# Optimization experiments

Hardware: AMD Instinct MI355X
Metric: run time of the kernel (lower is better)

## Reference

```python
import jax, jax.numpy as jnp
import numpy as np
import math

E = 512
H = 2048
P = 128  # attention_limit

def _make_params(key):
    ks = jax.random.split(key, 6)
    s = 0.02
    p = {}
    p['wq'] = jax.random.normal(ks[0], (E, E), jnp.float32) * s
    p['bq'] = jnp.zeros((E,), jnp.float32)
    p['wk'] = jax.random.normal(ks[1], (E, E), jnp.float32) * s
    p['bk'] = jnp.zeros((E,), jnp.float32)
    p['wv'] = jax.random.normal(ks[2], (E, E), jnp.float32) * s
    p['bv'] = jnp.zeros((E,), jnp.float32)
    p['w1'] = jax.random.normal(ks[3], (E, H), jnp.float32) * s
    p['b1'] = jnp.zeros((H,), jnp.float32)
    p['w2'] = jax.random.normal(ks[4], (H, E), jnp.float32) * s
    p['b2'] = jnp.zeros((E,), jnp.float32)
    p['ln1_w'] = jnp.ones((E,), jnp.float32)
    p['ln1_b'] = jnp.zeros((E,), jnp.float32)
    p['ln2_w'] = jnp.ones((E,), jnp.float32)
    p['ln2_b'] = jnp.zeros((E,), jnp.float32)
    return p

def setup_inputs() -> dict:
    key = jax.random.key(0)
    kx, kp = jax.random.split(key)
    inp = {'x': jax.random.normal(kx, (2, 1024, E), jnp.float32)}
    inp.update(_make_params(kp))
    return inp

def _layernorm(x, w, b, eps=1e-5):
    mu = jnp.mean(x, axis=-1, keepdims=True)
    var = jnp.mean((x - mu) ** 2, axis=-1, keepdims=True)
    return (x - mu) / jnp.sqrt(var + eps) * w + b

def _forward(x, wq, bq, wk, bk, wv, bv, w1, b1, w2, b2, ln1_w, ln1_b, ln2_w, ln2_b):
    B, S, Ed = x.shape
    # "RoPE" is actually additive sinusoidal PE in the source
    pos = jnp.arange(S, dtype=jnp.float32)[:, None]
    div = jnp.exp(jnp.arange(0, Ed, 2, dtype=jnp.float32) * (-math.log(10000.0) / Ed))
    pe = jnp.zeros((S, Ed), jnp.float32)
    pe = pe.at[:, 0::2].set(jnp.sin(pos * div))
    pe = pe.at[:, 1::2].set(jnp.cos(pos * div))
    x = x + pe[None]

    # local attention: pad x first, then apply K/V linears (padded rows -> bias)
    x_ext = jnp.pad(x, ((0, 0), (P, P), (0, 0)))
    q = x @ wq + bq                      # [B,S,E]
    k_ext = x_ext @ wk + bk              # [B,S+2P,E]
    v_ext = x_ext @ wv + bv
    W = 2 * P + 1
    win_idx = jnp.arange(S)[:, None] + jnp.arange(W)[None, :]  # [S,W]
    k_win = k_ext[:, win_idx]            # [B,S,W,E]
    v_win = v_ext[:, win_idx]            # [B,S,W,E]
    energy = jnp.einsum('bse,bswe->bsw', q, k_win) / jnp.sqrt(jnp.float32(Ed))
    attn = jax.nn.softmax(energy, axis=-1)
    attn_out = jnp.einsum('bsw,bswe->bse', attn, v_win)

    x = _layernorm(attn_out + x, ln1_w, ln1_b)
    ff = jnp.maximum(x @ w1 + b1, 0.0) @ w2 + b2
    return _layernorm(ff + x, ln2_w, ln2_b)

def reference(x, wq, bq, wk, bk, wv, bv, w1, b1, w2, b2, ln1_w, ln1_b, ln2_w, ln2_b):
    return _forward(x, wq, bq, wk, bk, wv, bv, w1, b1, w2, b2, ln1_w, ln1_b, ln2_w, ln2_b)
```

## Files before the change

kernel.cpp:

```cpp
#include <hip/hip_runtime.h>
#include <hip/hip_bf16.h>

#define S_LEN 1024
#define E_DIM 512
#define H_DIM 2048
#define EXTA 1296
#define BS_ROWS 2048

typedef __attribute__((ext_vector_type(8))) short bf16x8;
typedef __attribute__((ext_vector_type(4))) float f32x4;

__device__ inline ushort f2bf(float x) {
  union { float f; unsigned u; } c; c.f = x;
  unsigned u = c.u;
  u += 0x7fffu + ((u >> 16) & 1u);
  return (ushort)(u >> 16);
}
__device__ inline float bf2f(ushort u) {
  union { unsigned u; float f; } c;
  c.u = ((unsigned)u) << 16;
  return c.f;
}

__device__ inline void gload16(ushort* dst, const ushort* src) {
  __builtin_amdgcn_global_load_lds(
      (const __attribute__((address_space(1))) void*)src,
      (__attribute__((address_space(3))) void*)dst, 16, 0, 0);
}

__global__ __launch_bounds__(256) void prep_kernel(const float* __restrict__ x,
                                                   const float* __restrict__ wq,
                                                   const float* __restrict__ wk,
                                                   const float* __restrict__ wv,
                                                   const float* __restrict__ bk,
                                                   const float* __restrict__ bv,
                                                   ushort* __restrict__ xpe_bf,
                                                   ushort* __restrict__ wqkvT,
                                                   ushort* __restrict__ k_bf,
                                                   ushort* __restrict__ v_t) {
  __shared__ float t[32][33];
  const int blk = blockIdx.x;
  if (blk < 1024) {
    int idx = blk * 256 + threadIdx.x;
    int ep = idx & 255;
    int s = idx >> 8;
    int e0 = ep * 2;
    const float c = -9.210340371976184f / 512.0f;
    float freq = __expf((float)e0 * c);
    float sn, cs;
    __sincosf((float)s * freq, &sn, &cs);
    size_t base = (size_t)s * E_DIM + e0;
    float2 x0 = *(const float2*)(x + base);
    float2 x1 = *(const float2*)(x + base + S_LEN * E_DIM);
    ushort2 o0, o1;
    o0.x = f2bf(x0.x + sn); o0.y = f2bf(x0.y + cs);
    o1.x = f2bf(x1.x + sn); o1.y = f2bf(x1.y + cs);
    *(ushort2*)(xpe_bf + base) = o0;
    *(ushort2*)(xpe_bf + base + S_LEN * E_DIM) = o1;
  } else if (blk < 1792) {
    const int tile = blk - 1024;
    const int sect = tile >> 8, tt = tile & 255;
    const float* W = sect == 0 ? wq : (sect == 1 ? wk : wv);
    ushort* WT = wqkvT + (size_t)sect * 512 * 512;
    const int bx = tt & 15, by = tt >> 4;
    int lx = threadIdx.x & 31, ly = threadIdx.x >> 5;
    int n0 = bx * 32, k0 = by * 32;
#pragma unroll
    for (int r = 0; r < 4; ++r)
      t[ly + r * 8][lx] = W[(size_t)(k0 + ly + r * 8) * 512 + n0 + lx];
    __syncthreads();
#pragma unroll
    for (int r = 0; r < 4; ++r)
      WT[(size_t)(n0 + ly + r * 8) * 512 + k0 + lx] = f2bf(t[lx][ly + r * 8]);
  } else {
    int p = (blk - 1792) * 256 + threadIdx.x;
    int t2 = p / (2 * 272 * 512);
    int r2 = p % (2 * 272 * 512);
    int b = r2 / (272 * 512);
    int r3 = r2 % (272 * 512);
    if (t2 == 0) {
      int rr = r3 >> 9, e = r3 & 511;
      int row = rr < 128 ? rr : 1024 + rr;
      float v = rr < 256 ? bk[e] : 0.f;
      k_bf[((size_t)b * EXTA + row) * 512 + e] = f2bf(v);
    } else {
      int n = r3 / 272, jj = r3 % 272;
      int j = jj < 128 ? jj : 1024 + jj;
      float v = jj < 256 ? bv[n] : 0.f;
      v_t[((size_t)b * 512 + n) * EXTA + j] = f2bf(v);
    }
  }
}

__global__ __launch_bounds__(256, 4) void qkv_kernel(const ushort* __restrict__ A,
                                                     const ushort* __restrict__ Bt,
                                                     const float* __restrict__ bq,
                                                     const float* __restrict__ bk,
                                                     const float* __restrict__ bv,
                                                     ushort* __restrict__ q_out,
                                                     ushort* __restrict__ k_out,
                                                     ushort* __restrict__ v_out) {
  __shared__ ushort As[64 * 64];
  __shared__ ushort Bs[64 * 64];
  const int blk = blockIdx.x;
  const int tid = threadIdx.x;
  const int lane = tid & 63;
  const int w = tid >> 6;
  const int wr = w >> 1, wc = w & 1;
  const int l15 = lane & 15, lhi = lane >> 4;
  const int col0 = (blk % 24) * 64, row0 = (blk / 24) * 64;

  f32x4 acc[2][2] = {};

  for (int k0 = 0; k0 < 512; k0 += 64) {
#pragma unroll
    for (int it = 0; it < 2; ++it) {
      int u = it * 256 + tid;
      int r = u >> 3;
      int c16 = (u & 7) ^ (r & 7);
      gload16(&As[(size_t)u * 8], &A[(size_t)(row0 + r) * 512 + k0 + c16 * 8]);
    }
#pragma unroll
    for (int it = 0; it < 2; ++it) {
      int u = it * 256 + tid;
      int r = u >> 3;
      int c16 = (u & 7) ^ (r & 7);
      gload16(&Bs[(size_t)u * 8], &Bt[(size_t)(col0 + r) * 512 + k0 + c16 * 8]);
    }
    __syncthreads();
#pragma unroll
    for (int kk = 0; kk < 2; ++kk) {
      bf16x8 af[2], bfr[2];
#pragma unroll
      for (int mi = 0; mi < 2; ++mi) {
        int r = wr * 32 + mi * 16 + l15;
        int c16 = (kk * 4 + lhi) ^ (r & 7);
        af[mi] = *(const bf16x8*)&As[r * 64 + c16 * 8];
      }
#pragma unroll
      for (int ni = 0; ni < 2; ++ni) {
        int r = wc * 32 + ni * 16 + l15;
        int c16 = (kk * 4 + lhi) ^ (r & 7);
        bfr[ni] = *(const bf16x8*)&Bs[r * 64 + c16 * 8];
      }
#pragma unroll
      for (int mi = 0; mi < 2; ++mi)
#pragma unroll
        for (int ni = 0; ni < 2; ++ni)
          acc[mi][ni] = __builtin_amdgcn_mfma_f32_16x16x32_bf16(af[mi], bfr[ni], acc[mi][ni], 0, 0, 0);
    }
    __syncthreads();
  }

#pragma unroll
  for (int mi = 0; mi < 2; ++mi) {
    int mbase = row0 + wr * 32 + mi * 16 + lhi * 4;
#pragma unroll
    for (int ni = 0; ni < 2; ++ni) {
      int n = col0 + wc * 32 + ni * 16 + l15;
      int sect = n >> 9, nn = n & 511;
      float b = sect == 0 ? bq[nn] : (sect == 1 ? bk[nn] : bv[nn]);
      int bb = mbase >> 10;
      int s = mbase & 1023;
      if (sect == 0) {
#pragma unroll
        for (int j = 0; j < 4; ++j)
          q_out[(size_t)(mbase + j) * 512 + nn] = f2bf(acc[mi][ni][j] + b);
      } else if (sect == 1) {
#pragma unroll
        for (int j = 0; j < 4; ++j)
          k_out[((size_t)bb * EXTA + 128 + s + j) * 512 + nn] = f2bf(acc[mi][ni][j] + b);
      } else {
        ushort4 pk;
        pk.x = f2bf(acc[mi][ni][0] + b);
        pk.y = f2bf(acc[mi][ni][1] + b);
        pk.z = f2bf(acc[mi][ni][2] + b);
        pk.w = f2bf(acc[mi][ni][3] + b);
        *(ushort4*)&v_out[((size_t)bb * 512 + nn) * EXTA + 128 + s] = pk;
      }
    }
  }
}

template <int OUT>
__global__ __launch_bounds__(256, 4) void mfma_gemm(const ushort* __restrict__ A,
                                                    const ushort* __restrict__ Bt,
                                                    const float* __restrict__ bias,
                                                    void* __restrict__ Cout,
                                                    int M, int N, int K, int LDA) {
  __shared__ ushort As[64 * 64];
  __shared__ ushort Bs[64 * 64];
  const int tid = threadIdx.x;
  const int lane = tid & 63;
  const int w = tid >> 6;
  const int wr = w >> 1, wc = w & 1;
  const int l15 = lane & 15, lhi = lane >> 4;
  const int col0 = blockIdx.x * 64, row0 = blockIdx.y * 64;
  const int koff = blockIdx.z * K;

  f32x4 acc[2][2] = {};

  for (int k0 = 0; k0 < K; k0 += 64) {
#pragma unroll
    for (int it = 0; it < 2; ++it) {
      int u = it * 256 + tid;
      int r = u >> 3;
      int c16 = (u & 7) ^ (r & 7);
      gload16(&As[(size_t)u * 8], &A[(size_t)(row0 + r) * LDA + koff + k0 + c16 * 8]);
    }
#pragma unroll
    for (int it = 0; it < 2; ++it) {
      int u = it * 256 + tid;
      int r = u >> 3;
      int c16 = (u & 7) ^ (r & 7);
      gload16(&Bs[(size_t)u * 8], &Bt[(size_t)(col0 + r) * LDA + koff + k0 + c16 * 8]);
    }
    __syncthreads();
#pragma unroll
    for (int kk = 0; kk < 2; ++kk) {
      bf16x8 af[2], bfr[2];
#pragma unroll
      for (int mi = 0; mi < 2; ++mi) {
        int r = wr * 32 + mi * 16 + l15;
        int c16 = (kk * 4 + lhi) ^ (r & 7);
        af[mi] = *(const bf16x8*)&As[r * 64 + c16 * 8];
      }
#pragma unroll
      for (int ni = 0; ni < 2; ++ni) {
        int r = wc * 32 + ni * 16 + l15;
        int c16 = (kk * 4 + lhi) ^ (r & 7);
        bfr[ni] = *(const bf16x8*)&Bs[r * 64 + c16 * 8];
      }
#pragma unroll
      for (int mi = 0; mi < 2; ++mi)
#pragma unroll
        for (int ni = 0; ni < 2; ++ni)
          acc[mi][ni] = __builtin_amdgcn_mfma_f32_16x16x32_bf16(af[mi], bfr[ni], acc[mi][ni], 0, 0, 0);
    }
    __syncthreads();
  }

#pragma unroll
  for (int mi = 0; mi < 2; ++mi) {
    int mbase = row0 + wr * 32 + mi * 16 + lhi * 4;
#pragma unroll
    for (int ni = 0; ni < 2; ++ni) {
      int n = col0 + wc * 32 + ni * 16 + l15;
      if constexpr (OUT == 1) {
        float b = bias[n];
        ushort* C = (ushort*)Cout;
#pragma unroll
        for (int j = 0; j < 4; ++j)
          C[(size_t)(mbase + j) * N + n] = f2bf(fmaxf(acc[mi][ni][j] + b, 0.f));
      } else {
        float* C = (float*)Cout + (size_t)blockIdx.z * M * N;
#pragma unroll
        for (int j = 0; j < 4; ++j) C[(size_t)(mbase + j) * N + n] = acc[mi][ni][j];
      }
    }
  }
}

union AttnSm {
  struct {
    float e[16][292];
    ushort p[16][296];
    float inv[16];
    float redS[16][16];
    float redQ[16][16];
    float mu[16], rs[16];
  } a;
  float t[32][33];
};

__global__ __launch_bounds__(1024) void attn_ln1(const ushort* __restrict__ qb,
                                                 const ushort* __restrict__ kb,
                                                 const ushort* __restrict__ vt,
                                                 const ushort* __restrict__ xpe_bf,
                                                 const float* __restrict__ ln1w,
                                                 const float* __restrict__ ln1b,
                                                 const float* __restrict__ w1,
                                                 const float* __restrict__ w2,
                                                 ushort* __restrict__ w1T,
                                                 ushort* __restrict__ w2T,
                                                 ushort* __restrict__ x1bf) {
  __shared__ AttnSm sm;
  const int tid = threadIdx.x;

  if (blockIdx.x >= 128) {
    const int tile = blockIdx.x - 128;
    const float* W; ushort* WT; int K, N, bx, by;
    if (tile < 1024) {
      K = 512; N = 2048; W = w1; WT = w1T;
      bx = tile & 63; by = tile >> 6;
    } else {
      K = 2048; N = 512; W = w2; WT = w2T;
      int tt = tile - 1024; bx = tt & 15; by = tt >> 4;
    }
    int lx = tid & 31, ly = tid >> 5;
    int n0 = bx * 32, k0 = by * 32;
    sm.t[ly][lx] = W[(size_t)(k0 + ly) * N + n0 + lx];
    __syncthreads();
    WT[(size_t)(n0 + ly) * K + k0 + lx] = f2bf(sm.t[lx][ly]);
    return;
  }

  const int lane = tid & 63;
  const int w = tid >> 6;
  const int l15 = lane & 15, lhi = lane >> 4;
  const int tile = blockIdx.x;
  const int b = tile >> 6;
  const int s0 = (tile & 63) * 16;
  const int base0 = b * 1024 + s0;

  const ushort* qrow = qb + (size_t)(base0 + l15) * 512 + lhi * 8;
  bf16x8 qf[16];
#pragma unroll
  for (int ks = 0; ks < 16; ++ks) qf[ks] = *(const bf16x8*)(qrow + ks * 32);

  const float scale = 0.044194173824159216f;
  const ushort* kbase = kb + (size_t)b * EXTA * 512 + (size_t)(s0 + l15) * 512 + lhi * 8;

  for (int jt = w; jt < 18; jt += 16) {
    f32x4 acc = {};
    const ushort* kp = kbase + (size_t)jt * 16 * 512;
#pragma unroll
    for (int ks = 0; ks < 16; ++ks) {
      bf16x8 kf = *(const bf16x8*)(kp + ks * 32);
      acc = __builtin_amdgcn_mfma_f32_16x16x32_bf16(qf[ks], kf, acc, 0, 0, 0);
    }
    int jc = jt * 16 + l15;
#pragma unroll
    for (int j = 0; j < 4; ++j) {
      int i = lhi * 4 + j;
      bool valid = (jc >= i) && (jc <= i + 256);
      sm.a.e[i][jc] = valid ? acc[j] * scale : -1e30f;
    }
  }
  __syncthreads();

  {
    int r = w;
    float m = -1e30f;
#pragma unroll
    for (int t = 0; t < 5; ++t) {
      int col = lane + 64 * t;
      float e = (t < 4 || lane < 32) ? sm.a.e[r][col] : -1e30f;
      m = fmaxf(m, e);
    }
#pragma unroll
    for (int off = 1; off <= 32; off <<= 1) m = fmaxf(m, __shfl_xor(m, off));
    float s = 0.f;
#pragma unroll
    for (int t = 0; t < 5; ++t) {
      int col = lane + 64 * t;
      if (t < 4 || lane < 32) {
        float p = __expf(sm.a.e[r][col] - m);
        s += p;
        sm.a.p[r][col] = f2bf(p);
      }
    }
#pragma unroll
    for (int off = 1; off <= 32; off <<= 1) s += __shfl_xor(s, off);
    if (lane == 0) sm.a.inv[r] = 1.0f / s;
  }
  __syncthreads();

  bf16x8 pf[9];
#pragma unroll
  for (int ks = 0; ks < 9; ++ks) pf[ks] = *(const bf16x8*)&sm.a.p[l15][ks * 32 + lhi * 8];
  float inv[4];
#pragma unroll
  for (int j = 0; j < 4; ++j) inv[j] = sm.a.inv[lhi * 4 + j];

  const ushort* vbase = vt + (size_t)b * 512 * EXTA + s0 + lhi * 8;
  float val[2][4];
#pragma unroll
  for (int ni = 0; ni < 2; ++ni) {
    int n = w * 32 + ni * 16 + l15;
    f32x4 acc = {};
    const ushort* vp = vbase + (size_t)n * EXTA;
#pragma unroll
    for (int ks = 0; ks < 9; ++ks) {
      bf16x8 vf = *(const bf16x8*)(vp + ks * 32);
      acc = __builtin_amdgcn_mfma_f32_16x16x32_bf16(pf[ks], vf, acc, 0, 0, 0);
    }
#pragma unroll
    for (int j = 0; j < 4; ++j) {
      int r = lhi * 4 + j;
      val[ni][j] = acc[j] * inv[j] + bf2f(xpe_bf[(size_t)(base0 + r) * 512 + n]);
    }
  }

  float S[4], Q[4];
#pragma unroll
  for (int j = 0; j < 4; ++j) {
    S[j] = 0.f; Q[j] = 0.f;
#pragma unroll
    for (int ni = 0; ni < 2; ++ni) { S[j] += val[ni][j]; Q[j] += val[ni][j] * val[ni][j]; }
  }
#pragma unroll
  for (int off = 1; off <= 8; off <<= 1) {
#pragma unroll
    for (int j = 0; j < 4; ++j) {
      S[j] += __shfl_xor(S[j], off);
      Q[j] += __shfl_xor(Q[j], off);
    }
  }
  if (l15 == 0) {
#pragma unroll
    for (int j = 0; j < 4; ++j) { sm.a.redS[w][lhi * 4 + j] = S[j]; sm.a.redQ[w][lhi * 4 + j] = Q[j]; }
  }
  __syncthreads();
  if (tid < 16) {
    float sS = 0.f, sQ = 0.f;
#pragma unroll
    for (int ww = 0; ww < 16; ++ww) { sS += sm.a.redS[ww][tid]; sQ += sm.a.redQ[ww][tid]; }
    float mu = sS * (1.0f / 512.0f);
    float var = sQ * (1.0f / 512.0f) - mu * mu;
    sm.a.mu[tid] = mu;
    sm.a.rs[tid] = rsqrtf(var + 1e-5f);
  }
  __syncthreads();

#pragma unroll
  for (int ni = 0; ni < 2; ++ni) {
    int n = w * 32 + ni * 16 + l15;
    float lw = ln1w[n], lb = ln1b[n];
#pragma unroll
    for (int j = 0; j < 4; ++j) {
      int r = lhi * 4 + j;
      float o = (val[ni][j] - sm.a.mu[r]) * sm.a.rs[r] * lw + lb;
      x1bf[(size_t)(base0 + r) * 512 + n] = f2bf(o);
    }
  }
}

__device__ inline float wave_reduce_sum(float v) {
#pragma unroll
  for (int off = 32; off >= 1; off >>= 1) v += __shfl_xor(v, off);
  return v;
}

__global__ __launch_bounds__(256) void ln2_kernel(const float* __restrict__ parts,
                                                  const float* __restrict__ ab,
                                                  const ushort* __restrict__ rsd_bf,
                                                  const float* __restrict__ w,
                                                  const float* __restrict__ bias,
                                                  float* __restrict__ out) {
  const int row = blockIdx.x;
  const int tid = threadIdx.x;
  __shared__ float red[8];
  const int e0 = tid * 2;
  const size_t base = (size_t)row * E_DIM + e0;
  const size_t PART = (size_t)BS_ROWS * E_DIM;
  float2 v0 = *(const float2*)(parts + base);
  float2 v1 = *(const float2*)(parts + PART + base);
  float2 bb = *(const float2*)(ab + e0);
  ushort2 rv = *(const ushort2*)(rsd_bf + base);
  float x0 = v0.x + v1.x + bb.x + bf2f(rv.x);
  float x1 = v0.y + v1.y + bb.y + bf2f(rv.y);

  float sm = wave_reduce_sum(x0 + x1);
  if ((tid & 63) == 0) red[tid >> 6] = sm;
  __syncthreads();
  float mu = (red[0] + red[1] + red[2] + red[3]) * (1.0f / 512.0f);
  float d0 = x0 - mu, d1 = x1 - mu;
  float vs = wave_reduce_sum(d0 * d0 + d1 * d1);
  if ((tid & 63) == 0) red[4 + (tid >> 6)] = vs;
  __syncthreads();
  float var = (red[4] + red[5] + red[6] + red[7]) * (1.0f / 512.0f);
  float inv = rsqrtf(var + 1e-5f);
  float2 wv = *(const float2*)(w + e0);
  float2 bi = *(const float2*)(bias + e0);
  float o0 = d0 * inv * wv.x + bi.x;
  float o1 = d1 * inv * wv.y + bi.y;
  *(float2*)(out + base) = make_float2(o0, o1);
}

extern "C" void kernel_launch(void* const* d_in, const int* in_sizes, int n_in,
                              void* d_out, int out_size, void* d_ws, size_t ws_size,
                              hipStream_t stream) {
  const float* x    = (const float*)d_in[0];
  const float* wq   = (const float*)d_in[1];
  const float* bq   = (const float*)d_in[2];
  const float* wk   = (const float*)d_in[3];
  const float* bk   = (const float*)d_in[4];
  const float* wv   = (const float*)d_in[5];
  const float* bv   = (const float*)d_in[6];
  const float* w1   = (const float*)d_in[7];
  const float* b1   = (const float*)d_in[8];
  const float* w2   = (const float*)d_in[9];
  const float* b2   = (const float*)d_in[10];
  const float* ln1w = (const float*)d_in[11];
  const float* ln1b = (const float*)d_in[12];
  const float* ln2w = (const float*)d_in[13];
  const float* ln2b = (const float*)d_in[14];

  char* W = (char*)d_ws;
  ushort* xpebf  = (ushort*)(W);
  ushort* wqkvT  = (ushort*)(W + (2u  << 20));
  ushort* w1T    = (ushort*)(W + (4u  << 20));
  ushort* w2T    = (ushort*)(W + (6u  << 20));
  ushort* q_bf   = (ushort*)(W + (8u  << 20));
  ushort* k_bf   = (ushort*)(W + (10u << 20));
  ushort* v_t    = (ushort*)(W + (13u << 20));
  ushort* x1bf   = (ushort*)(W + (16u << 20));
  ushort* ff1_bf = (ushort*)(W + (18u << 20));
  float*  ff2    = (float*)(W + (26u << 20));

  prep_kernel<<<3968, 256, 0, stream>>>(x, wq, wk, wv, bk, bv,
                                        xpebf, wqkvT, k_bf, v_t);

  qkv_kernel<<<768, 256, 0, stream>>>(xpebf, wqkvT, bq, bk, bv, q_bf, k_bf, v_t);

  attn_ln1<<<2176, 1024, 0, stream>>>(q_bf, k_bf, v_t, xpebf, ln1w, ln1b,
                                      w1, w2, w1T, w2T, x1bf);

  mfma_gemm<1><<<dim3(32, 32), 256, 0, stream>>>(
      x1bf, w1T, b1, ff1_bf, BS_ROWS, H_DIM, 512, 512);

  mfma_gemm<3><<<dim3(8, 32, 2), 256, 0, stream>>>(
      ff1_bf, w2T, nullptr, ff2, BS_ROWS, E_DIM, 1024, 2048);

  ln2_kernel<<<BS_ROWS, 256, 0, stream>>>(ff2, b2, x1bf, ln2w, ln2b, (float*)d_out);
}
```

Baseline: 70.88 us.

## Double-buffer LDS tiles in QKV and MFMA GEMM kernels with async prefetch

Both GEMM kernels now use two LDS buffers per operand and issue the global-to-LDS loads for the next K tile before computing on the current one. An explicit vmcnt wait followed by a barrier replaces the single load-then-sync pattern, so memory latency can overlap with MFMA work. The change doubles LDS use per block (32KB), which may reduce occupancy under the 4-blocks launch bound. It also relies on gload16 being an asynchronous direct-to-LDS load counted by vmcnt.

```diff
diff --git a/kernel.cpp b/kernel.cpp
--- a/kernel.cpp
+++ b/kernel.cpp
@@ -100,8 +100,8 @@
                                                      ushort* __restrict__ q_out,
                                                      ushort* __restrict__ k_out,
                                                      ushort* __restrict__ v_out) {
-  __shared__ ushort As[64 * 64];
-  __shared__ ushort Bs[64 * 64];
+  __shared__ ushort As[2][64 * 64];
+  __shared__ ushort Bs[2][64 * 64];
   const int blk = blockIdx.x;
   const int tid = threadIdx.x;
   const int lane = tid & 63;
@@ -110,24 +110,31 @@
   const int l15 = lane & 15, lhi = lane >> 4;
   const int col0 = (blk % 24) * 64, row0 = (blk / 24) * 64;
 
+  int u0 = tid, u1 = 256 + tid;
+  int ra0 = u0 >> 3, ca0 = ((u0 & 7) ^ (ra0 & 7)) * 8;
+  int ra1 = u1 >> 3, ca1 = ((u1 & 7) ^ (ra1 & 7)) * 8;
+
   f32x4 acc[2][2] = {};
 
-  for (int k0 = 0; k0 < 512; k0 += 64) {
-#pragma unroll
-    for (int it = 0; it < 2; ++it) {
-      int u = it * 256 + tid;
-      int r = u >> 3;
-      int c16 = (u & 7) ^ (r & 7);
-      gload16(&As[(size_t)u * 8], &A[(size_t)(row0 + r) * 512 + k0 + c16 * 8]);
-    }
-#pragma unroll
-    for (int it = 0; it < 2; ++it) {
-      int u = it * 256 + tid;
-      int r = u >> 3;
-      int c16 = (u & 7) ^ (r & 7);
-      gload16(&Bs[(size_t)u * 8], &Bt[(size_t)(col0 + r) * 512 + k0 + c16 * 8]);
-    }
-    __syncthreads();
+  gload16(&As[0][u0 * 8], &A[(size_t)(row0 + ra0) * 512 + ca0]);
+  gload16(&As[0][u1 * 8], &A[(size_t)(row0 + ra1) * 512 + ca1]);
+  gload16(&Bs[0][u0 * 8], &Bt[(size_t)(col0 + ra0) * 512 + ca0]);
+  gload16(&Bs[0][u1 * 8], &Bt[(size_t)(col0 + ra1) * 512 + ca1]);
+
+  for (int t = 0; t < 8; ++t) {
+    const int cur = t & 1;
+    if (t < 7) {
+      int k0 = (t + 1) * 64;
+      gload16(&As[cur ^ 1][u0 * 8], &A[(size_t)(row0 + ra0) * 512 + k0 + ca0]);
+      gload16(&As[cur ^ 1][u1 * 8], &A[(size_t)(row0 + ra1) * 512 + k0 + ca1]);
+      gload16(&Bs[cur ^ 1][u0 * 8], &Bt[(size_t)(col0 + ra0) * 512 + k0 + ca0]);
+      gload16(&Bs[cur ^ 1][u1 * 8], &Bt[(size_t)(col0 + ra1) * 512 + k0 + ca1]);
+      asm volatile("s_waitcnt vmcnt(4)" ::: "memory");
+    } else {
+      asm volatile("s_waitcnt vmcnt(0)" ::: "memory");
+    }
+    __builtin_amdgcn_s_barrier();
+    __builtin_amdgcn_sched_barrier(0);
 #pragma unroll
     for (int kk = 0; kk < 2; ++kk) {
       bf16x8 af[2], bfr[2];
@@ -135,13 +142,13 @@
       for (int mi = 0; mi < 2; ++mi) {
         int r = wr * 32 + mi * 16 + l15;
         int c16 = (kk * 4 + lhi) ^ (r & 7);
-        af[mi] = *(const bf16x8*)&As[r * 64 + c16 * 8];
+        af[mi] = *(const bf16x8*)&As[cur][r * 64 + c16 * 8];
       }
 #pragma unroll
       for (int ni = 0; ni < 2; ++ni) {
         int r = wc * 32 + ni * 16 + l15;
         int c16 = (kk * 4 + lhi) ^ (r & 7);
-        bfr[ni] = *(const bf16x8*)&Bs[r * 64 + c16 * 8];
+        bfr[ni] = *(const bf16x8*)&Bs[cur][r * 64 + c16 * 8];
       }
 #pragma unroll
       for (int mi = 0; mi < 2; ++mi)
@@ -149,7 +156,8 @@
         for (int ni = 0; ni < 2; ++ni)
           acc[mi][ni] = __builtin_amdgcn_mfma_f32_16x16x32_bf16(af[mi], bfr[ni], acc[mi][ni], 0, 0, 0);
     }
-    __syncthreads();
+    __builtin_amdgcn_sched_barrier(0);
+    __builtin_amdgcn_s_barrier();
   }
 
 #pragma unroll
@@ -188,8 +196,8 @@
                                                     const float* __restrict__ bias,
                                                     void* __restrict__ Cout,
                                                     int M, int N, int K, int LDA) {
-  __shared__ ushort As[64 * 64];
-  __shared__ ushort Bs[64 * 64];
+  __shared__ ushort As[2][64 * 64];
+  __shared__ ushort Bs[2][64 * 64];
   const int tid = threadIdx.x;
   const int lane = tid & 63;
   const int w = tid >> 6;
@@ -197,25 +205,35 @@
   const int l15 = lane & 15, lhi = lane >> 4;
   const int col0 = blockIdx.x * 64, row0 = blockIdx.y * 64;
   const int koff = blockIdx.z * K;
+  const int nt = K >> 6;
+
+  int u0 = tid, u1 = 256 + tid;
+  int ra0 = u0 >> 3, ca0 = ((u0 & 7) ^ (ra0 & 7)) * 8;
+  int ra1 = u1 >> 3, ca1 = ((u1 & 7) ^ (ra1 & 7)) * 8;
+  const ushort* Abase = A + (size_t)row0 * LDA + koff;
+  const ushort* Bbase = Bt + (size_t)col0 * LDA + koff;
 
   f32x4 acc[2][2] = {};
 
-  for (int k0 = 0; k0 < K; k0 += 64) {
-#pragma unroll
-    for (int it = 0; it < 2; ++it) {
-      int u = it * 256 + tid;
-      int r = u >> 3;
-      int c16 = (u & 7) ^ (r & 7);
-      gload16(&As[(size_t)u * 8], &A[(size_t)(row0 + r) * LDA + koff + k0 + c16 * 8]);
-    }
-#pragma unroll
-    for (int it = 0; it < 2; ++it) {
-      int u = it * 256 + tid;
-      int r = u >> 3;
-      int c16 = (u & 7) ^ (r & 7);
-      gload16(&Bs[(size_t)u * 8], &Bt[(size_t)(col0 + r) * LDA + koff + k0 + c16 * 8]);
-    }
-    __syncthreads();
+  gload16(&As[0][u0 * 8], &Abase[(size_t)ra0 * LDA + ca0]);
+  gload16(&As[0][u1 * 8], &Abase[(size_t)ra1 * LDA + ca1]);
+  gload16(&Bs[0][u0 * 8], &Bbase[(size_t)ra0 * LDA + ca0]);
+  gload16(&Bs[0][u1 * 8], &Bbase[(size_t)ra1 * LDA + ca1]);
+
+  for (int t = 0; t < nt; ++t) {
+    const int cur = t & 1;
+    if (t + 1 < nt) {
+      int k0 = (t + 1) * 64;
+      gload16(&As[cur ^ 1][u0 * 8], &Abase[(size_t)ra0 * LDA + k0 + ca0]);
+      gload16(&As[cur ^ 1][u1 * 8], &Abase[(size_t)ra1 * LDA + k0 + ca1]);
+      gload16(&Bs[cur ^ 1][u0 * 8], &Bbase[(size_t)ra0 * LDA + k0 + ca0]);
+      gload16(&Bs[cur ^ 1][u1 * 8], &Bbase[(size_t)ra1 * LDA + k0 + ca1]);
+      asm volatile("s_waitcnt vmcnt(4)" ::: "memory");
+    } else {
+      asm volatile("s_waitcnt vmcnt(0)" ::: "memory");
+    }
+    __builtin_amdgcn_s_barrier();
+    __builtin_amdgcn_sched_barrier(0);
 #pragma unroll
     for (int kk = 0; kk < 2; ++kk) {
       bf16x8 af[2], bfr[2];
@@ -223,13 +241,13 @@
       for (int mi = 0; mi < 2; ++mi) {
         int r = wr * 32 + mi * 16 + l15;
         int c16 = (kk * 4 + lhi) ^ (r & 7);
-        af[mi] = *(const bf16x8*)&As[r * 64 + c16 * 8];
+        af[mi] = *(const bf16x8*)&As[cur][r * 64 + c16 * 8];
       }
 #pragma unroll
       for (int ni = 0; ni < 2; ++ni) {
         int r = wc * 32 + ni * 16 + l15;
         int c16 = (kk * 4 + lhi) ^ (r & 7);
-        bfr[ni] = *(const bf16x8*)&Bs[r * 64 + c16 * 8];
+        bfr[ni] = *(const bf16x8*)&Bs[cur][r * 64 + c16 * 8];
       }
 #pragma unroll
       for (int mi = 0; mi < 2; ++mi)
@@ -237,7 +255,8 @@
         for (int ni = 0; ni < 2; ++ni)
           acc[mi][ni] = __builtin_amdgcn_mfma_f32_16x16x32_bf16(af[mi], bfr[ni], acc[mi][ni], 0, 0, 0);
     }
-    __syncthreads();
+    __builtin_amdgcn_sched_barrier(0);
+    __builtin_amdgcn_s_barrier();
   }
 
 #pragma unroll
```

After: 71.37 us. About the same (+0.7%).
